# Kernel tuning notes

Hardware: AMD Instinct MI355X
Metric: run time of the kernel (lower is better)

## Reference

```python
import jax, jax.numpy as jnp
import numpy as np

LAM = 0.5


def _conv3x3(z, W):
    # z: [n, 2, h, w], W: [1, 2, 3, 3] (OIHW), padding=1, no bias
    return jax.lax.conv_general_dilated(
        z, W, window_strides=(1, 1), padding='SAME',
        dimension_numbers=('NCHW', 'OIHW', 'NCHW'))


def setup_inputs() -> dict:
    key = jax.random.key(0)
    k0, k1, k2, k3 = jax.random.split(key, 4)
    n, t, c, h, w = 32, 8, 128, 32, 32
    x = jax.random.normal(k0, (n, t, c, h, w), dtype=jnp.float32)
    alpha = jnp.full((1,), 0.5, dtype=jnp.float32)
    beta = jnp.full((1,), 0.5, dtype=jnp.float32)
    W_fc = jax.random.normal(k1, (t, t), dtype=jnp.float32) * (1.0 / np.sqrt(t))
    W_conv1 = jax.random.normal(k2, (1, 2, 3, 3), dtype=jnp.float32) * 0.2
    W_conv2 = jax.random.normal(k3, (1, 2, 3, 3), dtype=jnp.float32) * 0.2
    return {"x": x, "alpha": alpha, "beta": beta, "W_fc": W_fc,
            "W_conv1": W_conv1, "W_conv2": W_conv2}


def reference(x, alpha, beta, W_fc, W_conv1, W_conv2):
    n, t, c, h, w = x.shape
    # --- pooled time-channel map ---
    avg = jnp.mean(x, axis=(3, 4))            # [n,t,c]
    mx = jnp.max(x, axis=(3, 4))              # [n,t,c]
    map_add = 0.5 * (avg + mx) + alpha[0] * avg + beta[0] * mx
    # fc along time axis (Linear(t,t,bias=False) applied to [n,c,t]):
    # y[n,s,c] = sum_t map_add[n,t,c] * W_fc[s,t]
    map_add = jnp.einsum('ntc,st->nsc', map_add, W_fc)  # [n,t,c]

    kc = int(c * LAM)
    kt = int(t * LAM)
    # important channels: topk over channel axis, per timestep.
    # Faithful to the original: the fancy-index assignment unions the topk
    # selections over the batch, so the mask is batch-independent.
    _, idx_c = jax.lax.top_k(map_add, kc)                     # [n,t,kc]
    mask_c = jax.nn.one_hot(idx_c, c, dtype=x.dtype).max(axis=2).max(axis=0)  # [t,c]
    # important times: topk over time axis, per channel.
    _, idx_t = jax.lax.top_k(jnp.swapaxes(map_add, 1, 2), kt)  # [n,c,kt]
    mask_t = jax.nn.one_hot(idx_t, t, dtype=x.dtype).max(axis=2).max(axis=0).T  # [t,c]

    # torch.where((mask_c+mask_t)/2 == 0.5, 1, 0)  ==  XOR of the two masks
    im_tc = ((mask_c + mask_t) == 1.0).astype(x.dtype)  # [t,c]
    sub_tc = 1.0 - im_tc

    imf = x * im_tc[None, :, :, None, None]
    subf = x * sub_tc[None, :, :, None, None]
    imf = imf.reshape(n, t * c, h, w)
    subf = subf.reshape(n, t * c, h, w)

    im_avg = jnp.mean(imf, axis=1, keepdims=True) / LAM
    im_max = jnp.max(imf, axis=1, keepdims=True)
    sub_avg = jnp.mean(subf, axis=1, keepdims=True) / (1.0 - LAM)
    sub_max = jnp.max(subf, axis=1, keepdims=True)

    im_map = jax.nn.sigmoid(_conv3x3(jnp.concatenate([im_avg, im_max], axis=1), W_conv1))
    sub_map = jax.nn.sigmoid(_conv3x3(jnp.concatenate([sub_avg, sub_max], axis=1), W_conv2))

    out = im_map * imf + sub_map * subf                 # [n, t*c, h, w]
    return out.reshape(n, t, c, h, w)
```

## Files before the change

### kernel.cpp

```cpp
#include <hip/hip_runtime.h>
#include <math.h>

#define TC  1024
#define P_  1024
#define KC  64
#define KT  4


__global__ __launch_bounds__(256) void k1_reduce(const float* __restrict__ x,
                                                 float* __restrict__ avg,
                                                 float* __restrict__ mx,
                                                 int* __restrict__ masks) {
    int r = blockIdx.x;
    if (r == 0) {
        #pragma unroll
        for (int j = 0; j < 8; ++j) masks[j * 256 + threadIdx.x] = 0;
    }
    const float4* xp = (const float4*)(x + (size_t)r * P_);
    float4 v = xp[threadIdx.x];
    float s = (v.x + v.y) + (v.z + v.w);
    float m = fmaxf(fmaxf(v.x, v.y), fmaxf(v.z, v.w));
    #pragma unroll
    for (int off = 32; off > 0; off >>= 1) {
        s += __shfl_down(s, off);
        m  = fmaxf(m, __shfl_down(m, off));
    }
    __shared__ float ss[4], sm[4];
    int wid = threadIdx.x >> 6, lane = threadIdx.x & 63;
    if (lane == 0) { ss[wid] = s; sm[wid] = m; }
    __syncthreads();
    if (threadIdx.x == 0) {
        float ts = (ss[0] + ss[1]) + (ss[2] + ss[3]);
        float tm = fmaxf(fmaxf(sm[0], sm[1]), fmaxf(sm[2], sm[3]));
        avg[r] = ts * (1.0f / 1024.0f);
        mx[r]  = tm;
    }
}

__global__ __launch_bounds__(256) void k2_map(const float* __restrict__ avg,
                                              const float* __restrict__ mx,
                                              const float* __restrict__ alpha,
                                              const float* __restrict__ beta,
                                              const float* __restrict__ wfc,
                                              int* __restrict__ mask_c,
                                              int* __restrict__ mask_t) {
    __shared__ float m[TC], mf[TC], w[64];
    int n = blockIdx.x;
    float a0 = alpha[0], b0 = beta[0];
    if (threadIdx.x < 64) w[threadIdx.x] = wfc[threadIdx.x];
    for (int i = threadIdx.x; i < TC; i += 256) {
        float a = avg[n * TC + i], b = mx[n * TC + i];
        m[i] = 0.5f * (a + b) + a0 * a + b0 * b;
    }
    __syncthreads();
    for (int i = threadIdx.x; i < TC; i += 256) {
        int s = i >> 7, cc = i & 127;
        float acc = 0.0f;
        #pragma unroll
        for (int tt = 0; tt < 8; ++tt) acc += m[tt * 128 + cc] * w[s * 8 + tt];
        mf[i] = acc;
    }
    __syncthreads();
    for (int i = threadIdx.x; i < TC; i += 256) {
        int tt = i >> 7, cc = i & 127;
        float v = mf[i];
        int rc = 0;
        #pragma unroll 16
        for (int c2 = 0; c2 < 128; ++c2) {
            float u = mf[tt * 128 + c2];
            rc += (u > v) || (u == v && c2 < cc);
        }
        if (rc < KC) mask_c[i] = 1;
        int rt = 0;
        #pragma unroll
        for (int t2 = 0; t2 < 8; ++t2) {
            float u = mf[t2 * 128 + cc];
            rt += (u > v) || (u == v && t2 < tt);
        }
        if (rt < KT) mask_t[i] = 1;
    }
}

__global__ __launch_bounds__(256) void k4_partial(const float* __restrict__ x,
                                                  const int* __restrict__ mask_c,
                                                  const int* __restrict__ mask_t,
                                                  float* __restrict__ flag_out,
                                                  float* __restrict__ part) {
    int b = blockIdx.x;
    int kq = b & 3, g = (b >> 2) & 7, n = b >> 5;
    __shared__ float sf[128];
    if (threadIdx.x < 128) {
        int ch = g * 128 + threadIdx.x;
        float f = ((mask_c[ch] != 0) != (mask_t[ch] != 0)) ? 1.0f : 0.0f;
        sf[threadIdx.x] = f;
        if (n == 0 && kq == 0) flag_out[ch] = f;
    }
    __syncthreads();
    const float4* xb = (const float4*)x
                     + ((size_t)(n * TC + g * 128 + kq * 32) * 256) + threadIdx.x;
    float4 ims  = {0.f, 0.f, 0.f, 0.f};
    float4 subs = {0.f, 0.f, 0.f, 0.f};
    float4 imm  = {-INFINITY, -INFINITY, -INFINITY, -INFINITY};
    float4 subm = {-INFINITY, -INFINITY, -INFINITY, -INFINITY};
    #pragma unroll 8
    for (int k = 0; k < 32; ++k) {
        float4 v = xb[(size_t)k * 256];
        float f = sf[kq * 32 + k];
        float iv;
        iv = v.x * f; ims.x += iv; imm.x = fmaxf(imm.x, iv);
        v.x -= iv;    subs.x += v.x; subm.x = fmaxf(subm.x, v.x);
        iv = v.y * f; ims.y += iv; imm.y = fmaxf(imm.y, iv);
        v.y -= iv;    subs.y += v.y; subm.y = fmaxf(subm.y, v.y);
        iv = v.z * f; ims.z += iv; imm.z = fmaxf(imm.z, iv);
        v.z -= iv;    subs.z += v.z; subm.z = fmaxf(subm.z, v.z);
        iv = v.w * f; ims.w += iv; imm.w = fmaxf(imm.w, iv);
        v.w -= iv;    subs.w += v.w; subm.w = fmaxf(subm.w, v.w);
    }
    float4* pp = (float4*)part + (size_t)b * 256 + threadIdx.x;
    pp[0]      = ims;
    pp[262144] = imm;
    pp[524288] = subs;
    pp[786432] = subm;
}

__global__ __launch_bounds__(1024) void k5_conv(const float* __restrict__ part,
                                                const float* __restrict__ w1,
                                                const float* __restrict__ w2,
                                                float* __restrict__ im_map,
                                                float* __restrict__ sub_map) {
    __shared__ float sp[4][P_];
    int n = blockIdx.x, p = threadIdx.x;
    float s_im = 0.f, s_sub = 0.f, m_im = -INFINITY, m_sub = -INFINITY;
    #pragma unroll 8
    for (int gk = 0; gk < 32; ++gk) {
        size_t idx = ((size_t)(n * 32 + gk)) * P_ + p;
        s_im  += part[idx];
        m_im   = fmaxf(m_im, part[idx + 1048576]);
        s_sub += part[idx + 2097152];
        m_sub  = fmaxf(m_sub, part[idx + 3145728]);
    }
    sp[0][p] = (s_im  * (1.0f / 1024.0f)) / 0.5f;
    sp[1][p] = m_im;
    sp[2][p] = (s_sub * (1.0f / 1024.0f)) / 0.5f;
    sp[3][p] = m_sub;
    __syncthreads();
    int y = p >> 5, xx = p & 31;
    float acc1 = 0.0f, acc2 = 0.0f;
    #pragma unroll
    for (int i = 0; i < 2; ++i)
        #pragma unroll
        for (int dy = 0; dy < 3; ++dy) {
            int yy = y + dy - 1;
            if (yy < 0 || yy >= 32) continue;
            #pragma unroll
            for (int dx = 0; dx < 3; ++dx) {
                int xc = xx + dx - 1;
                if (xc < 0 || xc >= 32) continue;
                acc1 += sp[i][yy * 32 + xc]     * w1[i * 9 + dy * 3 + dx];
                acc2 += sp[2 + i][yy * 32 + xc] * w2[i * 9 + dy * 3 + dx];
            }
        }
    im_map[n * P_ + p]  = 1.0f / (1.0f + expf(-acc1));
    sub_map[n * P_ + p] = 1.0f / (1.0f + expf(-acc2));
}

__global__ __launch_bounds__(256) void k6_out(const float* __restrict__ x,
                                              const float* __restrict__ flag,
                                              const float* __restrict__ im_map,
                                              const float* __restrict__ sub_map,
                                              float* __restrict__ out) {
    size_t i4 = (size_t)blockIdx.x * 256 + threadIdx.x;
    size_t e = i4 * 4;
    int n   = (int)(e >> 20);
    int rem = (int)(e & 1048575);
    int ch  = rem >> 10;
    int pix = rem & 1023;
    float4 xv = ((const float4*)x)[i4];
    bool im = flag[ch] != 0.0f;
    const float* mp = (im ? im_map : sub_map) + (size_t)n * P_ + pix;
    float4 mv = *(const float4*)mp;
    float4 o;
    o.x = xv.x * mv.x; o.y = xv.y * mv.y; o.z = xv.z * mv.z; o.w = xv.w * mv.w;
    ((float4*)out)[i4] = o;
}

extern "C" void kernel_launch(void* const* d_in, const int* in_sizes, int n_in,
                              void* d_out, int out_size, void* d_ws, size_t ws_size,
                              hipStream_t stream) {
    const float* x     = (const float*)d_in[0];
    const float* alpha = (const float*)d_in[1];
    const float* beta  = (const float*)d_in[2];
    const float* wfc   = (const float*)d_in[3];
    const float* w1    = (const float*)d_in[4];
    const float* w2    = (const float*)d_in[5];
    float* out = (float*)d_out;
    float* ws  = (float*)d_ws;

    float* avg     = ws;
    float* mx      = ws + 32768;
    int*   mask_c  = (int*)(ws + 65536);
    int*   mask_t  = (int*)(ws + 66560);
    float* flag    = ws + 67584;
    float* im_map  = ws + 68608;
    float* sub_map = ws + 101376;
    float* part    = ws + 134144;

    k1_reduce <<<32768, 256, 0, stream>>>(x, avg, mx, mask_c);
    k2_map    <<<32,    256, 0, stream>>>(avg, mx, alpha, beta, wfc, mask_c, mask_t);
    k4_partial<<<1024,  256, 0, stream>>>(x, mask_c, mask_t, flag, part);
    k5_conv   <<<32,   1024, 0, stream>>>(part, w1, w2, im_map, sub_map);
    k6_out    <<<32768, 256, 0, stream>>>(x, flag, im_map, sub_map, out);
}
```

Baseline: 115.7 us.

## Rebalance top-k, partial-reduction, and output kernels across blocks

k2_map now runs one block per (batch, timestep) instead of one per batch, spreading the rank computation over 8x more blocks. k4_partial is restructured so each block covers a quarter of the pixels and a quarter of the channels, and its four waves reduce through shared memory before writing. This shrinks the partial buffer and the loop in k5_conv from 32 to 4 reads per pixel. k6_out handles four channels per thread, reusing the loaded map vectors, and writes output with nontemporal stores.

```diff
diff --git a/kernel.cpp b/kernel.cpp
--- a/kernel.cpp
+++ b/kernel.cpp
@@ -5,6 +5,8 @@
 #define P_  1024
 #define KC  64
 #define KT  4
+
+typedef float vfloat4 __attribute__((ext_vector_type(4)));
 
 
 __global__ __launch_bounds__(256) void k1_reduce(const float* __restrict__ x,
@@ -45,7 +47,7 @@
                                               int* __restrict__ mask_c,
                                               int* __restrict__ mask_t) {
     __shared__ float m[TC], mf[TC], w[64];
-    int n = blockIdx.x;
+    int n = blockIdx.x >> 3, tt = blockIdx.x & 7;
     float a0 = alpha[0], b0 = beta[0];
     if (threadIdx.x < 64) w[threadIdx.x] = wfc[threadIdx.x];
     for (int i = threadIdx.x; i < TC; i += 256) {
@@ -57,12 +59,12 @@
         int s = i >> 7, cc = i & 127;
         float acc = 0.0f;
         #pragma unroll
-        for (int tt = 0; tt < 8; ++tt) acc += m[tt * 128 + cc] * w[s * 8 + tt];
+        for (int t2 = 0; t2 < 8; ++t2) acc += m[t2 * 128 + cc] * w[s * 8 + t2];
         mf[i] = acc;
     }
     __syncthreads();
-    for (int i = threadIdx.x; i < TC; i += 256) {
-        int tt = i >> 7, cc = i & 127;
+    if (threadIdx.x < 128) {
+        int cc = threadIdx.x, i = tt * 128 + cc;
         float v = mf[i];
         int rc = 0;
         #pragma unroll 16
@@ -87,25 +89,29 @@
                                                   float* __restrict__ flag_out,
                                                   float* __restrict__ part) {
     int b = blockIdx.x;
-    int kq = b & 3, g = (b >> 2) & 7, n = b >> 5;
-    __shared__ float sf[128];
-    if (threadIdx.x < 128) {
-        int ch = g * 128 + threadIdx.x;
+    int cq = b & 3, pq = (b >> 2) & 3, n = b >> 4;
+    __shared__ float sf[256];
+    __shared__ float4 red[4][4][64];
+    {
+        int i = threadIdx.x;
+        int ch = cq * 256 + i;
         float f = ((mask_c[ch] != 0) != (mask_t[ch] != 0)) ? 1.0f : 0.0f;
-        sf[threadIdx.x] = f;
-        if (n == 0 && kq == 0) flag_out[ch] = f;
-    }
-    __syncthreads();
-    const float4* xb = (const float4*)x
-                     + ((size_t)(n * TC + g * 128 + kq * 32) * 256) + threadIdx.x;
+        sf[i] = f;
+        if (n == 0 && pq == 0) flag_out[ch] = f;
+    }
+    __syncthreads();
+    int l = threadIdx.x & 63, cg = threadIdx.x >> 6;
+    int f4p = pq * 64 + l;
+    int ch0 = cq * 256 + cg * 64;
+    const float4* xb = (const float4*)x + ((size_t)(n * TC + ch0)) * 256 + f4p;
     float4 ims  = {0.f, 0.f, 0.f, 0.f};
     float4 subs = {0.f, 0.f, 0.f, 0.f};
     float4 imm  = {-INFINITY, -INFINITY, -INFINITY, -INFINITY};
     float4 subm = {-INFINITY, -INFINITY, -INFINITY, -INFINITY};
     #pragma unroll 8
-    for (int k = 0; k < 32; ++k) {
+    for (int k = 0; k < 64; ++k) {
         float4 v = xb[(size_t)k * 256];
-        float f = sf[kq * 32 + k];
+        float f = sf[cg * 64 + k];
         float iv;
         iv = v.x * f; ims.x += iv; imm.x = fmaxf(imm.x, iv);
         v.x -= iv;    subs.x += v.x; subm.x = fmaxf(subm.x, v.x);
@@ -116,11 +122,29 @@
         iv = v.w * f; ims.w += iv; imm.w = fmaxf(imm.w, iv);
         v.w -= iv;    subs.w += v.w; subm.w = fmaxf(subm.w, v.w);
     }
-    float4* pp = (float4*)part + (size_t)b * 256 + threadIdx.x;
-    pp[0]      = ims;
-    pp[262144] = imm;
-    pp[524288] = subs;
-    pp[786432] = subm;
+    red[0][cg][l] = ims;
+    red[1][cg][l] = imm;
+    red[2][cg][l] = subs;
+    red[3][cg][l] = subm;
+    __syncthreads();
+    if (threadIdx.x < 64) {
+        float4 s0 = red[0][0][l], s1 = red[1][0][l], s2 = red[2][0][l], s3 = red[3][0][l];
+        #pragma unroll
+        for (int g = 1; g < 4; ++g) {
+            float4 a = red[0][g][l], bq = red[1][g][l], c = red[2][g][l], d = red[3][g][l];
+            s0.x += a.x; s0.y += a.y; s0.z += a.z; s0.w += a.w;
+            s1.x = fmaxf(s1.x, bq.x); s1.y = fmaxf(s1.y, bq.y);
+            s1.z = fmaxf(s1.z, bq.z); s1.w = fmaxf(s1.w, bq.w);
+            s2.x += c.x; s2.y += c.y; s2.z += c.z; s2.w += c.w;
+            s3.x = fmaxf(s3.x, d.x); s3.y = fmaxf(s3.y, d.y);
+            s3.z = fmaxf(s3.z, d.z); s3.w = fmaxf(s3.w, d.w);
+        }
+        float4* pp = (float4*)part + ((size_t)(cq * 32 + n) * 4) * 256 + f4p;
+        pp[0]   = s0;
+        pp[256] = s1;
+        pp[512] = s2;
+        pp[768] = s3;
+    }
 }
 
 __global__ __launch_bounds__(1024) void k5_conv(const float* __restrict__ part,
@@ -131,17 +155,17 @@
     __shared__ float sp[4][P_];
     int n = blockIdx.x, p = threadIdx.x;
     float s_im = 0.f, s_sub = 0.f, m_im = -INFINITY, m_sub = -INFINITY;
-    #pragma unroll 8
-    for (int gk = 0; gk < 32; ++gk) {
-        size_t idx = ((size_t)(n * 32 + gk)) * P_ + p;
-        s_im  += part[idx];
-        m_im   = fmaxf(m_im, part[idx + 1048576]);
-        s_sub += part[idx + 2097152];
-        m_sub  = fmaxf(m_sub, part[idx + 3145728]);
-    }
-    sp[0][p] = (s_im  * (1.0f / 1024.0f)) / 0.5f;
+    #pragma unroll
+    for (int q = 0; q < 4; ++q) {
+        size_t base = ((size_t)(q * 32 + n) * 4) * P_ + p;
+        s_im  += part[base];
+        m_im   = fmaxf(m_im, part[base + 1024]);
+        s_sub += part[base + 2048];
+        m_sub  = fmaxf(m_sub, part[base + 3072]);
+    }
+    sp[0][p] = s_im  * (2.0f / 1024.0f);
     sp[1][p] = m_im;
-    sp[2][p] = (s_sub * (1.0f / 1024.0f)) / 0.5f;
+    sp[2][p] = s_sub * (2.0f / 1024.0f);
     sp[3][p] = m_sub;
     __syncthreads();
     int y = p >> 5, xx = p & 31;
@@ -169,19 +193,26 @@
                                               const float* __restrict__ im_map,
                                               const float* __restrict__ sub_map,
                                               float* __restrict__ out) {
-    size_t i4 = (size_t)blockIdx.x * 256 + threadIdx.x;
-    size_t e = i4 * 4;
-    int n   = (int)(e >> 20);
-    int rem = (int)(e & 1048575);
-    int ch  = rem >> 10;
-    int pix = rem & 1023;
-    float4 xv = ((const float4*)x)[i4];
-    bool im = flag[ch] != 0.0f;
-    const float* mp = (im ? im_map : sub_map) + (size_t)n * P_ + pix;
-    float4 mv = *(const float4*)mp;
-    float4 o;
-    o.x = xv.x * mv.x; o.y = xv.y * mv.y; o.z = xv.z * mv.z; o.w = xv.w * mv.w;
-    ((float4*)out)[i4] = o;
+    int g   = blockIdx.x * 256 + threadIdx.x;
+    int n   = g >> 16;
+    int rem = g & 65535;
+    int ch    = rem >> 8;
+    int pixf4 = rem & 255;
+    size_t base = ((size_t)n << 18) + rem;
+    const float4* xp = (const float4*)x + base;
+    const float4* imb  = (const float4*)im_map  + n * 256 + pixf4;
+    const float4* subb = (const float4*)sub_map + n * 256 + pixf4;
+    float4 im_v  = *imb;
+    float4 sub_v = *subb;
+    #pragma unroll
+    for (int j = 0; j < 4; ++j) {
+        float4 xv = xp[j * 65536];
+        bool im = flag[ch + j * 256] != 0.0f;
+        float4 mv = im ? im_v : sub_v;
+        vfloat4 o;
+        o.x = xv.x * mv.x; o.y = xv.y * mv.y; o.z = xv.z * mv.z; o.w = xv.w * mv.w;
+        __builtin_nontemporal_store(o, (vfloat4*)out + base + (size_t)j * 65536);
+    }
 }
 
 extern "C" void kernel_launch(void* const* d_in, const int* in_sizes, int n_in,
@@ -206,8 +237,8 @@
     float* part    = ws + 134144;
 
     k1_reduce <<<32768, 256, 0, stream>>>(x, avg, mx, mask_c);
-    k2_map    <<<32,    256, 0, stream>>>(avg, mx, alpha, beta, wfc, mask_c, mask_t);
-    k4_partial<<<1024,  256, 0, stream>>>(x, mask_c, mask_t, flag, part);
+    k2_map    <<<256,   256, 0, stream>>>(avg, mx, alpha, beta, wfc, mask_c, mask_t);
+    k4_partial<<<512,   256, 0, stream>>>(x, mask_c, mask_t, flag, part);
     k5_conv   <<<32,   1024, 0, stream>>>(part, w1, w2, im_map, sub_map);
-    k6_out    <<<32768, 256, 0, stream>>>(x, flag, im_map, sub_map, out);
-}
+    k6_out    <<<8192,  256, 0, stream>>>(x, flag, im_map, sub_map, out);
+}
```

After: 96.59 us. 16.5% less time.
